# Kernel tuning notes

Measured on AMD Instinct MI355X. Metric: run time of the kernel, lower is better.

The kernel has to match this reference:

```python
import jax, jax.numpy as jnp
import numpy as np

N = 100  # n_subcritics; +-1/+-10 neighbor offsets imply a fixed 10x10 grid
OFFSETS = np.array([0, -10, 1, 10, -1])  # neighbor order: (i, i-10, i+1, i+10, i-1)


def _neighbor_gather(x):
    # x: [B, T, N, 7] -> xi: [B, T, N, 35]; out-of-range neighbors contribute zeros
    idx = np.arange(N)[:, None] + OFFSETS[None, :]          # [N, 5]
    mask = (idx >= 0) & (idx < N)
    idx_c = np.clip(idx, 0, N - 1)
    g = x[:, :, idx_c, :] * jnp.asarray(mask, x.dtype)[None, None, :, :, None]
    return g.reshape(x.shape[0], x.shape[1], N, 5 * x.shape[-1])


def _forward(x, lm_W1, lm_b1, lm_W2, lm_b2, lm_W3, lm_b3,
             gru_Wih, gru_Whh, gru_bih, gru_bhh,
             sc_W1, sc_b1, sc_W2, sc_b2, sc_W3, sc_b3):
    xi = _neighbor_gather(x)                                 # [B, T, N, 35]
    # LocalizedModule (per-node MLP) on the last timestep
    xl = xi[:, -1]                                           # [B, N, 35]
    h = jax.nn.relu(jnp.einsum('bnf,nfh->bnh', xl, lm_W1) + lm_b1)
    h = jax.nn.relu(jnp.einsum('bnf,nfh->bnh', h, lm_W2) + lm_b2)
    f = jnp.einsum('bnf,nfo->bno', h, lm_W3) + lm_b3         # [B, N, 1]
    # SubCritic: per-node GRU (PyTorch gate order r, z, n) over time, then MLP on final hidden
    def step(hc, xt):
        gi = jnp.einsum('bnf,ngf->bng', xt, gru_Wih) + gru_bih   # [B, N, 48]
        gh = jnp.einsum('bnh,ngh->bng', hc, gru_Whh) + gru_bhh
        ir, iz, i_n = jnp.split(gi, 3, axis=-1)
        hr, hz, h_n = jnp.split(gh, 3, axis=-1)
        r = jax.nn.sigmoid(ir + hr)
        z = jax.nn.sigmoid(iz + hz)
        n = jnp.tanh(i_n + r * h_n)
        return (1.0 - z) * n + z * hc, None
    h0 = jnp.zeros((x.shape[0], N, gru_Whh.shape[-1]), x.dtype)
    hT, _ = jax.lax.scan(step, h0, jnp.moveaxis(xi, 1, 0))   # final hidden [B, N, 16]
    g = jax.nn.relu(jnp.einsum('bnf,nfh->bnh', hT, sc_W1) + sc_b1)
    g = jax.nn.relu(jnp.einsum('bnf,nfh->bnh', g, sc_W2) + sc_b2)
    q = jnp.einsum('bnf,nfo->bno', g, sc_W3) + sc_b3         # [B, N, 1]
    # torch.cat over node-major lists of [B,1] then sum(dim=1) -> [N*B]
    return jnp.transpose(f[..., 0] + q[..., 0]).reshape(-1)


def setup_inputs():
    key = jax.random.key(0)
    ks = jax.random.split(key, 18)
    B, T, S, G = 128, 256, 7, 16
    def w(k, shape, scale=0.05):
        return jax.random.normal(k, shape, dtype=jnp.float32) * scale
    return {
        'x': jax.random.normal(ks[0], (B, T, N, S), dtype=jnp.float32),
        'lm_W1': w(ks[1], (N, 35, 512)), 'lm_b1': w(ks[2], (N, 512)),
        'lm_W2': w(ks[3], (N, 512, 256)), 'lm_b2': w(ks[4], (N, 256)),
        'lm_W3': w(ks[5], (N, 256, 1)), 'lm_b3': w(ks[6], (N, 1)),
        'gru_Wih': w(ks[7], (N, 3 * G, 35)), 'gru_Whh': w(ks[8], (N, 3 * G, G)),
        'gru_bih': w(ks[9], (N, 3 * G)), 'gru_bhh': w(ks[10], (N, 3 * G)),
        'sc_W1': w(ks[11], (N, G, G)), 'sc_b1': w(ks[12], (N, G)),
        'sc_W2': w(ks[13], (N, G, G)), 'sc_b2': w(ks[14], (N, G)),
        'sc_W3': w(ks[15], (N, G, 1)), 'sc_b3': w(ks[16], (N, 1)),
    }


def reference(x, lm_W1, lm_b1, lm_W2, lm_b2, lm_W3, lm_b3,
              gru_Wih, gru_Whh, gru_bih, gru_bhh,
              sc_W1, sc_b1, sc_W2, sc_b2, sc_W3, sc_b3):
    return _forward(x, lm_W1, lm_b1, lm_W2, lm_b2, lm_W3, lm_b3,
                    gru_Wih, gru_Whh, gru_bih, gru_bhh,
                    sc_W1, sc_b1, sc_W2, sc_b2, sc_W3, sc_b3)
```

## Files before the change

kernel.cpp:

```cpp
#include <hip/hip_runtime.h>
#include <cstddef>

#define NN 100
#define TT 256
#define BB 128
#define SS 7
#define FF 35
#define GG 16

typedef __attribute__((ext_vector_type(4))) float f32x4;
typedef __attribute__((ext_vector_type(8))) short short8;

__constant__ int c_off[5] = {0, -10, 1, 10, -1};

__device__ __forceinline__ float sigmoidf_(float v) {
  return __builtin_amdgcn_rcpf(1.0f + __expf(-v));
}
__device__ __forceinline__ float tanhf_(float v) {
  return 1.0f - 2.0f * __builtin_amdgcn_rcpf(__expf(2.0f * v) + 1.0f);
}
__device__ __forceinline__ unsigned bf1(float a) {
  unsigned u = __float_as_uint(a);
  return (u + 0x7FFFu + ((u >> 16) & 1u)) >> 16;
}
__device__ __forceinline__ unsigned bfp(float lo, float hi) {
  return bf1(lo) | (bf1(hi) << 16);
}
__device__ __forceinline__ unsigned pkt(float lo, float hi) {
  return (__float_as_uint(lo) >> 16) | (__float_as_uint(hi) & 0xFFFF0000u);
}

__global__ void __launch_bounds__(512)
k_lm1(const float* __restrict__ x, const float* __restrict__ W1,
      const float* __restrict__ b1, float* __restrict__ H1) {
  const int bc = blockIdx.x;
  const int n  = blockIdx.y;
  const int b0 = bc * 32;
  const int tid = threadIdx.x;
  __shared__ __align__(16) float xl[32][36];
  for (int idx = tid; idx < 32 * FF; idx += 512) {
    const int bb = idx / FF, f = idx % FF;
    const int m = n + c_off[f / SS];
    const int s = f % SS;
    float v = 0.0f;
    if (m >= 0 && m < NN)
      v = x[(((size_t)(b0 + bb) * TT + (TT - 1)) * NN + m) * SS + s];
    xl[bb][f] = v;
  }
  __syncthreads();
  const int h = tid;
  float w[FF];
  const float* wp = W1 + (size_t)n * FF * 512 + h;
#pragma unroll
  for (int f = 0; f < FF; ++f) w[f] = wp[(size_t)f * 512];
  const float bias = b1[n * 512 + h];
  for (int bb = 0; bb < 32; ++bb) {
    const float4* xr = (const float4*)(&xl[bb][0]);
    float acc = bias;
#pragma unroll
    for (int q = 0; q < 8; ++q) {
      const float4 v = xr[q];
      acc += w[4*q+0] * v.x + w[4*q+1] * v.y + w[4*q+2] * v.z + w[4*q+3] * v.w;
    }
    {
      const float4 v = xr[8];
      acc += w[32] * v.x + w[33] * v.y + w[34] * v.z;
    }
    H1[((size_t)(b0 + bb) * NN + n) * 512 + h] = fmaxf(acc, 0.0f);
  }
}

__global__ void __launch_bounds__(256)
k_lm2(const float* __restrict__ H1, const float* __restrict__ W2,
      const float* __restrict__ bias2, float* __restrict__ H2) {
  const int w  = threadIdx.x >> 6;
  const int l  = threadIdx.x & 63;
  const int n  = blockIdx.x >> 5;
  const int tg = blockIdx.x & 31;
  const int tau = tg * 4 + w;
  const int rt = tau >> 4;
  const int ct = tau & 15;
  const int lr = l & 15;
  const int kg = l >> 4;

  const int arow = rt * 16 + lr;
  const int col  = ct * 16 + lr;

  const float* Ab = H1 + ((size_t)arow * NN + n) * 512 + kg * 8;
  const float* Bb = W2 + (size_t)n * 512 * 256 + (size_t)(kg * 8) * 256 + col;

  f32x4 acc = {0.0f, 0.0f, 0.0f, 0.0f};
#pragma unroll 2
  for (int k0 = 0; k0 < 512; k0 += 32) {
    const float4 a0 = *(const float4*)(Ab + k0);
    const float4 a1 = *(const float4*)(Ab + k0 + 4);
    const float* bp = Bb + (size_t)k0 * 256;
    const float w0 = bp[0],    w1 = bp[256],  w2 = bp[512],  w3 = bp[768];
    const float w4 = bp[1024], w5 = bp[1280], w6 = bp[1536], w7 = bp[1792];
    union { short8 s; unsigned u[4]; } A, B;
    A.u[0] = pkt(a0.x, a0.y); A.u[1] = pkt(a0.z, a0.w);
    A.u[2] = pkt(a1.x, a1.y); A.u[3] = pkt(a1.z, a1.w);
    B.u[0] = pkt(w0, w1); B.u[1] = pkt(w2, w3);
    B.u[2] = pkt(w4, w5); B.u[3] = pkt(w6, w7);
    acc = __builtin_amdgcn_mfma_f32_16x16x32_bf16(A.s, B.s, acc, 0, 0, 0);
  }
  const float bv = bias2[n * 256 + col];
#pragma unroll
  for (int r = 0; r < 4; ++r) {
    const int grow = rt * 16 + kg * 4 + r;
    H2[((size_t)grow * NN + n) * 256 + col] = fmaxf(acc[r] + bv, 0.0f);
  }
}

__global__ void __launch_bounds__(256)
k_lm3(const float* __restrict__ H2, const float* __restrict__ W3,
      const float* __restrict__ b3, float* __restrict__ out) {
  const int w = threadIdx.x >> 6;
  const int lane = threadIdx.x & 63;
  const int p = blockIdx.x * 4 + w;
  const int b = p / NN, n = p % NN;
  const float4 hv = *(const float4*)(&H2[((size_t)b * NN + n) * 256 + lane*4]);
  const float4 wv = *(const float4*)(&W3[n * 256 + lane*4]);
  float dot = hv.x*wv.x + hv.y*wv.y + hv.z*wv.z + hv.w*wv.w;
#pragma unroll
  for (int off = 32; off > 0; off >>= 1) dot += __shfl_down(dot, off);
  if (lane == 0) out[n * BB + b] = dot + b3[n];
}

__device__ __forceinline__ float dot16s(const float4 u0, const float4 u1,
                                        const float4 u2, const float4 u3,
                                        const float4 h0, const float4 h1,
                                        const float4 h2, const float4 h3) {
  const float p0 = u0.x*h0.x + u0.y*h0.y + u0.z*h0.z + u0.w*h0.w;
  const float p1 = u1.x*h1.x + u1.y*h1.y + u1.z*h1.z + u1.w*h1.w;
  const float p2 = u2.x*h2.x + u2.y*h2.y + u2.z*h2.z + u2.w*h2.w;
  const float p3 = u3.x*h3.x + u3.y*h3.y + u3.z*h3.z + u3.w*h3.w;
  return (p0 + p1) + (p2 + p3);
}

__global__ void __launch_bounds__(64, 3)
k_gru(const float* __restrict__ x,
      const float* __restrict__ Wih, const float* __restrict__ Whh,
      const float* __restrict__ bih, const float* __restrict__ bhh,
      const float* __restrict__ sW1, const float* __restrict__ sb1,
      const float* __restrict__ sW2, const float* __restrict__ sb2,
      const float* __restrict__ sW3, const float* __restrict__ sb3,
      float* __restrict__ out) {
  const int l  = threadIdx.x;
  const int g  = l & 15;
  const int b  = l >> 4;
  const int kg = b;
  const int ab = (l & 15) >> 2;
  const int atoff = l & 3;
  const int bc = blockIdx.x;
  const int n  = blockIdx.y;
  const int bga = bc*4 + ab;
  const int bgp = bc*4 + b;

  __shared__ float hlds[4][16];

  const float* wh = Whh + ((size_t)n*48 + g)*GG;
  const float4 ur0 = *(const float4*)(wh+0),  ur1 = *(const float4*)(wh+4),
               ur2 = *(const float4*)(wh+8),  ur3 = *(const float4*)(wh+12);
  const float4 uz0 = *(const float4*)(wh+256),  uz1 = *(const float4*)(wh+260),
               uz2 = *(const float4*)(wh+264),  uz3 = *(const float4*)(wh+268);
  const float4 un0 = *(const float4*)(wh+512),  un1 = *(const float4*)(wh+516),
               un2 = *(const float4*)(wh+520),  un3 = *(const float4*)(wh+524);
  const float bir = bih[n*48 + g], biz = bih[n*48 + 16 + g], bin_ = bih[n*48 + 32 + g];
  const float bhr = bhh[n*48 + g], bhz = bhh[n*48 + 16 + g], bhn = bhh[n*48 + 32 + g];

  short8 bw[3], bw2[3];
#pragma unroll
  for (int c = 0; c < 3; ++c) {
    const float* wp = Wih + ((size_t)n*48 + c*16 + g)*FF;
    float t0_[8], t1_[8];
#pragma unroll
    for (int j = 0; j < 8; ++j) t0_[j] = wp[kg*8 + j];
#pragma unroll
    for (int j = 0; j < 8; ++j) {
      const int k2 = 32 + kg*8 + j;
      t1_[j] = (k2 < FF) ? wp[k2] : 0.0f;
    }
    union { short8 s; unsigned u[4]; } U, V;
#pragma unroll
    for (int jj = 0; jj < 4; ++jj) { U.u[jj] = bfp(t0_[2*jj], t0_[2*jj+1]);
                                     V.u[jj] = bfp(t1_[2*jj], t1_[2*jj+1]); }
    bw[c] = U.s; bw2[c] = V.s;
  }

  int adelta[8]; unsigned amask = 0;
#pragma unroll
  for (int j = 0; j < 8; ++j) {
    const int f  = kg*8 + j;
    const int fi = (f * 586) >> 12;
    const int s  = f - fi*7;
    const int mo = (fi == 0) ? 0 : (fi == 1) ? -10 : (fi == 2) ? 1 : (fi == 3) ? 10 : -1;
    adelta[j] = mo*SS + s;
    const int m = n + mo;
    if (m >= 0 && m < NN) amask |= (1u << j);
  }
  const bool v2 = (kg == 0) && (n >= 1);

  float xv[8], xv2[3];
  {
    const float* xq = x + ((size_t)bga*TT + atoff)*(NN*SS) + n*SS;
#pragma unroll
    for (int j = 0; j < 8; ++j) xv[j] = ((amask >> j) & 1u) ? xq[adelta[j]] : 0.0f;
#pragma unroll
    for (int j = 0; j < 3; ++j) xv2[j] = v2 ? xq[-3 + j] : 0.0f;
  }

  hlds[b][g] = 0.0f;
  float hown = 0.0f;

  const f32x4 z4 = {0.0f, 0.0f, 0.0f, 0.0f};

  for (int rd = 0; rd < TT/4; ++rd) {
    union { short8 s; unsigned u[4]; } A1, A2;
#pragma unroll
    for (int jj = 0; jj < 4; ++jj) A1.u[jj] = pkt(xv[2*jj], xv[2*jj+1]);
    A2.u[0] = pkt(xv2[0], xv2[1]); A2.u[1] = pkt(xv2[2], 0.0f); A2.u[2] = 0; A2.u[3] = 0;
    const short8 af1 = A1.s, af2 = A2.s;

    if (rd < TT/4 - 1) {
      const float* xq = x + ((size_t)bga*TT + (rd*4 + 4 + atoff))*(NN*SS) + n*SS;
#pragma unroll
      for (int j = 0; j < 8; ++j) xv[j] = ((amask >> j) & 1u) ? xq[adelta[j]] : 0.0f;
#pragma unroll
      for (int j = 0; j < 3; ++j) xv2[j] = v2 ? xq[-3 + j] : 0.0f;
    }

    f32x4 c0 = __builtin_amdgcn_mfma_f32_16x16x32_bf16(af1, bw[0], z4, 0, 0, 0);
    c0 = __builtin_amdgcn_mfma_f32_16x16x32_bf16(af2, bw2[0], c0, 0, 0, 0);
    f32x4 c1 = __builtin_amdgcn_mfma_f32_16x16x32_bf16(af1, bw[1], z4, 0, 0, 0);
    c1 = __builtin_amdgcn_mfma_f32_16x16x32_bf16(af2, bw2[1], c1, 0, 0, 0);
    f32x4 c2 = __builtin_amdgcn_mfma_f32_16x16x32_bf16(af1, bw[2], z4, 0, 0, 0);
    c2 = __builtin_amdgcn_mfma_f32_16x16x32_bf16(af2, bw2[2], c2, 0, 0, 0);

#pragma unroll
    for (int toff = 0; toff < 4; ++toff) {
      const float ir  = c0[toff] + bir;
      const float iz  = c1[toff] + biz;
      const float in_ = c2[toff] + bin_;
      const float4* hp = (const float4*)(&hlds[b][0]);
      const float4 h0 = hp[0], h1 = hp[1], h2 = hp[2], h3 = hp[3];
      const float hr = bhr + dot16s(ur0, ur1, ur2, ur3, h0, h1, h2, h3);
      const float hz = bhz + dot16s(uz0, uz1, uz2, uz3, h0, h1, h2, h3);
      const float hn = bhn + dot16s(un0, un1, un2, un3, h0, h1, h2, h3);
      const float r   = sigmoidf_(ir + hr);
      const float z   = sigmoidf_(iz + hz);
      const float nn2 = tanhf_(in_ + r * hn);
      const float hnew = nn2 + z * (hown - nn2);
      hlds[b][g] = hnew;
      hown = hnew;
    }
  }

  {
    const float4* hp = (const float4*)(&hlds[b][0]);
    const float4 h0 = hp[0], h1 = hp[1], h2 = hp[2], h3 = hp[3];
    const float* w1 = sW1 + n*GG*GG + g;
    float a1 = sb1[n*GG + g];
    a1 += h0.x*w1[0*GG] + h0.y*w1[1*GG] + h0.z*w1[2*GG] + h0.w*w1[3*GG];
    a1 += h1.x*w1[4*GG] + h1.y*w1[5*GG] + h1.z*w1[6*GG] + h1.w*w1[7*GG];
    a1 += h2.x*w1[8*GG] + h2.y*w1[9*GG] + h2.z*w1[10*GG] + h2.w*w1[11*GG];
    a1 += h3.x*w1[12*GG] + h3.y*w1[13*GG] + h3.z*w1[14*GG] + h3.w*w1[15*GG];
    a1 = fmaxf(a1, 0.0f);
    hlds[b][g] = a1;
  }
  {
    const float4* hp = (const float4*)(&hlds[b][0]);
    const float4 h0 = hp[0], h1 = hp[1], h2 = hp[2], h3 = hp[3];
    const float* w2 = sW2 + n*GG*GG + g;
    float a2 = sb2[n*GG + g];
    a2 += h0.x*w2[0*GG] + h0.y*w2[1*GG] + h0.z*w2[2*GG] + h0.w*w2[3*GG];
    a2 += h1.x*w2[4*GG] + h1.y*w2[5*GG] + h1.z*w2[6*GG] + h1.w*w2[7*GG];
    a2 += h2.x*w2[8*GG] + h2.y*w2[9*GG] + h2.z*w2[10*GG] + h2.w*w2[11*GG];
    a2 += h3.x*w2[12*GG] + h3.y*w2[13*GG] + h3.z*w2[14*GG] + h3.w*w2[15*GG];
    a2 = fmaxf(a2, 0.0f);
    float p = a2 * sW3[n*GG + g];
    p += __shfl_xor(p, 1);
    p += __shfl_xor(p, 2);
    p += __shfl_xor(p, 4);
    p += __shfl_xor(p, 8);
    if (g == 0) out[n * BB + bgp] += p + sb3[n];
  }
}

extern "C" void kernel_launch(void* const* d_in, const int* in_sizes, int n_in,
                              void* d_out, int out_size, void* d_ws, size_t ws_size,
                              hipStream_t stream) {
  const float* x     = (const float*)d_in[0];
  const float* lm_W1 = (const float*)d_in[1];
  const float* lm_b1 = (const float*)d_in[2];
  const float* lm_W2 = (const float*)d_in[3];
  const float* lm_b2 = (const float*)d_in[4];
  const float* lm_W3 = (const float*)d_in[5];
  const float* lm_b3 = (const float*)d_in[6];
  const float* gWih  = (const float*)d_in[7];
  const float* gWhh  = (const float*)d_in[8];
  const float* gbih  = (const float*)d_in[9];
  const float* gbhh  = (const float*)d_in[10];
  const float* sW1   = (const float*)d_in[11];
  const float* sb1   = (const float*)d_in[12];
  const float* sW2   = (const float*)d_in[13];
  const float* sb2   = (const float*)d_in[14];
  const float* sW3   = (const float*)d_in[15];
  const float* sb3   = (const float*)d_in[16];
  float* out = (float*)d_out;

  float* H1 = (float*)d_ws;
  float* H2 = (float*)((char*)d_ws + (size_t)BB * NN * 512 * 4);

  k_lm1<<<dim3(4, NN), 512, 0, stream>>>(x, lm_W1, lm_b1, H1);
  k_lm2<<<dim3(3200), 256, 0, stream>>>(H1, lm_W2, lm_b2, H2);
  k_lm3<<<dim3(3200), 256, 0, stream>>>(H2, lm_W3, lm_b3, out);
  k_gru<<<dim3(32, NN), 64, 0, stream>>>(x, gWih, gWhh, gbih, gbhh,
                                         sW1, sb1, sW2, sb2, sW3, sb3, out);
}
```

Baseline: 542.4 us.

## Tile lm2 GEMM through shared memory and broadcast GRU hidden state via DPP

```diff
diff --git a/kernel.cpp b/kernel.cpp
--- a/kernel.cpp
+++ b/kernel.cpp
@@ -29,6 +29,10 @@
 __device__ __forceinline__ unsigned pkt(float lo, float hi) {
   return (__float_as_uint(lo) >> 16) | (__float_as_uint(hi) & 0xFFFF0000u);
 }
+
+#define RORF(dst, src, J)                                                     \
+  dst = __uint_as_float(__builtin_amdgcn_update_dpp(                          \
+      0, (int)__float_as_uint(src), 0x120 + (J), 0xF, 0xF, true));
 
 __global__ void __launch_bounds__(512)
 k_lm1(const float* __restrict__ x, const float* __restrict__ W1,
@@ -73,42 +77,64 @@
 __global__ void __launch_bounds__(256)
 k_lm2(const float* __restrict__ H1, const float* __restrict__ W2,
       const float* __restrict__ bias2, float* __restrict__ H2) {
-  const int w  = threadIdx.x >> 6;
-  const int l  = threadIdx.x & 63;
-  const int n  = blockIdx.x >> 5;
-  const int tg = blockIdx.x & 31;
-  const int tau = tg * 4 + w;
-  const int rt = tau >> 4;
-  const int ct = tau & 15;
+  const int n  = blockIdx.x;
+  const int bh = blockIdx.y >> 2;
+  const int ch = blockIdx.y & 3;
+  const int t  = threadIdx.x;
+  const int w  = t >> 6;
+  const int l  = t & 63;
   const int lr = l & 15;
   const int kg = l >> 4;
-
-  const int arow = rt * 16 + lr;
-  const int col  = ct * 16 + lr;
-
-  const float* Ab = H1 + ((size_t)arow * NN + n) * 512 + kg * 8;
-  const float* Bb = W2 + (size_t)n * 512 * 256 + (size_t)(kg * 8) * 256 + col;
-
-  f32x4 acc = {0.0f, 0.0f, 0.0f, 0.0f};
-#pragma unroll 2
-  for (int k0 = 0; k0 < 512; k0 += 32) {
-    const float4 a0 = *(const float4*)(Ab + k0);
-    const float4 a1 = *(const float4*)(Ab + k0 + 4);
-    const float* bp = Bb + (size_t)k0 * 256;
-    const float w0 = bp[0],    w1 = bp[256],  w2 = bp[512],  w3 = bp[768];
-    const float w4 = bp[1024], w5 = bp[1280], w6 = bp[1536], w7 = bp[1792];
-    union { short8 s; unsigned u[4]; } A, B;
-    A.u[0] = pkt(a0.x, a0.y); A.u[1] = pkt(a0.z, a0.w);
-    A.u[2] = pkt(a1.x, a1.y); A.u[3] = pkt(a1.z, a1.w);
-    B.u[0] = pkt(w0, w1); B.u[1] = pkt(w2, w3);
-    B.u[2] = pkt(w4, w5); B.u[3] = pkt(w6, w7);
-    acc = __builtin_amdgcn_mfma_f32_16x16x32_bf16(A.s, B.s, acc, 0, 0, 0);
-  }
-  const float bv = bias2[n * 256 + col];
+  const int m0 = (w >> 1) * 32;
+  const int c0 = (w & 1) * 32;
+
+  __shared__ __align__(16) unsigned short As[64][72];
+
+  f32x4 acc00 = {0,0,0,0}, acc01 = {0,0,0,0}, acc10 = {0,0,0,0}, acc11 = {0,0,0,0};
+
+  const int colg0 = ch * 64 + c0;
+  const float* Bbase = W2 + (size_t)n * 512 * 256;
+
+  for (int k0 = 0; k0 < 512; k0 += 64) {
+    __syncthreads();
+#pragma unroll
+    for (int q = 0; q < 4; ++q) {
+      const int idx = t + q * 256;
+      const int row = idx >> 4;
+      const int kq  = idx & 15;
+      const float4 v = *(const float4*)(&H1[((size_t)(bh*64 + row) * NN + n) * 512 + k0 + kq*4]);
+      uint2 pv; pv.x = pkt(v.x, v.y); pv.y = pkt(v.z, v.w);
+      *(uint2*)(&As[row][kq*4]) = pv;
+    }
+    __syncthreads();
+#pragma unroll
+    for (int kc = 0; kc < 2; ++kc) {
+      const short8 a0 = *(const short8*)(&As[m0 + lr][kc*32 + kg*8]);
+      const short8 a1 = *(const short8*)(&As[m0 + 16 + lr][kc*32 + kg*8]);
+      union { short8 s; unsigned u[4]; } B0, B1;
+      const float* bp0 = Bbase + (size_t)(k0 + kc*32 + kg*8) * 256 + colg0 + lr;
+      const float* bp1 = bp0 + 16;
+#pragma unroll
+      for (int jj = 0; jj < 4; ++jj) {
+        B0.u[jj] = pkt(bp0[(size_t)(2*jj)*256], bp0[(size_t)(2*jj+1)*256]);
+        B1.u[jj] = pkt(bp1[(size_t)(2*jj)*256], bp1[(size_t)(2*jj+1)*256]);
+      }
+      acc00 = __builtin_amdgcn_mfma_f32_16x16x32_bf16(a0, B0.s, acc00, 0, 0, 0);
+      acc01 = __builtin_amdgcn_mfma_f32_16x16x32_bf16(a0, B1.s, acc01, 0, 0, 0);
+      acc10 = __builtin_amdgcn_mfma_f32_16x16x32_bf16(a1, B0.s, acc10, 0, 0, 0);
+      acc11 = __builtin_amdgcn_mfma_f32_16x16x32_bf16(a1, B1.s, acc11, 0, 0, 0);
+    }
+  }
+  const int colA = colg0 + lr, colB = colA + 16;
+  const float bva = bias2[n*256 + colA], bvb = bias2[n*256 + colB];
 #pragma unroll
   for (int r = 0; r < 4; ++r) {
-    const int grow = rt * 16 + kg * 4 + r;
-    H2[((size_t)grow * NN + n) * 256 + col] = fmaxf(acc[r] + bv, 0.0f);
+    const int rowA = bh*64 + m0 + kg*4 + r;
+    const int rowB = rowA + 16;
+    H2[((size_t)rowA * NN + n) * 256 + colA] = fmaxf(acc00[r] + bva, 0.0f);
+    H2[((size_t)rowA * NN + n) * 256 + colB] = fmaxf(acc01[r] + bvb, 0.0f);
+    H2[((size_t)rowB * NN + n) * 256 + colA] = fmaxf(acc10[r] + bva, 0.0f);
+    H2[((size_t)rowB * NN + n) * 256 + colB] = fmaxf(acc11[r] + bvb, 0.0f);
   }
 }
 
@@ -125,17 +151,6 @@
 #pragma unroll
   for (int off = 32; off > 0; off >>= 1) dot += __shfl_down(dot, off);
   if (lane == 0) out[n * BB + b] = dot + b3[n];
-}
-
-__device__ __forceinline__ float dot16s(const float4 u0, const float4 u1,
-                                        const float4 u2, const float4 u3,
-                                        const float4 h0, const float4 h1,
-                                        const float4 h2, const float4 h3) {
-  const float p0 = u0.x*h0.x + u0.y*h0.y + u0.z*h0.z + u0.w*h0.w;
-  const float p1 = u1.x*h1.x + u1.y*h1.y + u1.z*h1.z + u1.w*h1.w;
-  const float p2 = u2.x*h2.x + u2.y*h2.y + u2.z*h2.z + u2.w*h2.w;
-  const float p3 = u3.x*h3.x + u3.y*h3.y + u3.z*h3.z + u3.w*h3.w;
-  return (p0 + p1) + (p2 + p3);
 }
 
 __global__ void __launch_bounds__(64, 3)
@@ -157,15 +172,18 @@
   const int bga = bc*4 + ab;
   const int bgp = bc*4 + b;
 
-  __shared__ float hlds[4][16];
-
-  const float* wh = Whh + ((size_t)n*48 + g)*GG;
-  const float4 ur0 = *(const float4*)(wh+0),  ur1 = *(const float4*)(wh+4),
-               ur2 = *(const float4*)(wh+8),  ur3 = *(const float4*)(wh+12);
-  const float4 uz0 = *(const float4*)(wh+256),  uz1 = *(const float4*)(wh+260),
-               uz2 = *(const float4*)(wh+264),  uz3 = *(const float4*)(wh+268);
-  const float4 un0 = *(const float4*)(wh+512),  un1 = *(const float4*)(wh+516),
-               un2 = *(const float4*)(wh+520),  un3 = *(const float4*)(wh+524);
+  const int wpr = __builtin_amdgcn_update_dpp(0, g, 0x121, 0xF, 0xF, true);
+  const int s   = (wpr == ((g + 15) & 15)) ? -1 : 1;
+
+  const float* whr = Whh + ((size_t)n*48 +      g) * GG;
+  const float* whz = Whh + ((size_t)n*48 + 16 + g) * GG;
+  const float* whn = Whh + ((size_t)n*48 + 32 + g) * GG;
+  float ur[16], uz[16], un[16];
+#pragma unroll
+  for (int j = 0; j < 16; ++j) {
+    const int ix = (g + s*j) & 15;
+    ur[j] = whr[ix]; uz[j] = whz[ix]; un[j] = whn[ix];
+  }
   const float bir = bih[n*48 + g], biz = bih[n*48 + 16 + g], bin_ = bih[n*48 + 32 + g];
   const float bhr = bhh[n*48 + g], bhz = bhh[n*48 + 16 + g], bhn = bhh[n*48 + 32 + g];
 
@@ -181,11 +199,11 @@
       const int k2 = 32 + kg*8 + j;
       t1_[j] = (k2 < FF) ? wp[k2] : 0.0f;
     }
-    union { short8 s; unsigned u[4]; } U, V;
+    union { short8 s8; unsigned u[4]; } U, V;
 #pragma unroll
     for (int jj = 0; jj < 4; ++jj) { U.u[jj] = bfp(t0_[2*jj], t0_[2*jj+1]);
                                      V.u[jj] = bfp(t1_[2*jj], t1_[2*jj+1]); }
-    bw[c] = U.s; bw2[c] = V.s;
+    bw[c] = U.s8; bw2[c] = V.s8;
   }
 
   int adelta[8]; unsigned amask = 0;
@@ -193,9 +211,9 @@
   for (int j = 0; j < 8; ++j) {
     const int f  = kg*8 + j;
     const int fi = (f * 586) >> 12;
-    const int s  = f - fi*7;
+    const int sg = f - fi*7;
     const int mo = (fi == 0) ? 0 : (fi == 1) ? -10 : (fi == 2) ? 1 : (fi == 3) ? 10 : -1;
-    adelta[j] = mo*SS + s;
+    adelta[j] = mo*SS + sg;
     const int m = n + mo;
     if (m >= 0 && m < NN) amask |= (1u << j);
   }
@@ -210,17 +228,15 @@
     for (int j = 0; j < 3; ++j) xv2[j] = v2 ? xq[-3 + j] : 0.0f;
   }
 
-  hlds[b][g] = 0.0f;
   float hown = 0.0f;
-
   const f32x4 z4 = {0.0f, 0.0f, 0.0f, 0.0f};
 
   for (int rd = 0; rd < TT/4; ++rd) {
-    union { short8 s; unsigned u[4]; } A1, A2;
+    union { short8 s8; unsigned u[4]; } A1, A2;
 #pragma unroll
     for (int jj = 0; jj < 4; ++jj) A1.u[jj] = pkt(xv[2*jj], xv[2*jj+1]);
     A2.u[0] = pkt(xv2[0], xv2[1]); A2.u[1] = pkt(xv2[2], 0.0f); A2.u[2] = 0; A2.u[3] = 0;
-    const short8 af1 = A1.s, af2 = A2.s;
+    const short8 af1 = A1.s8, af2 = A2.s8;
 
     if (rd < TT/4 - 1) {
       const float* xq = x + ((size_t)bga*TT + (rd*4 + 4 + atoff))*(NN*SS) + n*SS;
@@ -239,45 +255,75 @@
 
 #pragma unroll
     for (int toff = 0; toff < 4; ++toff) {
-      const float ir  = c0[toff] + bir;
-      const float iz  = c1[toff] + biz;
-      const float in_ = c2[toff] + bin_;
-      const float4* hp = (const float4*)(&hlds[b][0]);
-      const float4 h0 = hp[0], h1 = hp[1], h2 = hp[2], h3 = hp[3];
-      const float hr = bhr + dot16s(ur0, ur1, ur2, ur3, h0, h1, h2, h3);
-      const float hz = bhz + dot16s(uz0, uz1, uz2, uz3, h0, h1, h2, h3);
-      const float hn = bhn + dot16s(un0, un1, un2, un3, h0, h1, h2, h3);
-      const float r   = sigmoidf_(ir + hr);
-      const float z   = sigmoidf_(iz + hz);
-      const float nn2 = tanhf_(in_ + r * hn);
-      const float hnew = nn2 + z * (hown - nn2);
-      hlds[b][g] = hnew;
-      hown = hnew;
-    }
-  }
-
+      float h1, h2, h3, h4, h5, h6, h7, h8, h9, h10, h11, h12, h13, h14, h15;
+      RORF(h1,  hown, 1)  RORF(h2,  hown, 2)  RORF(h3,  hown, 3)
+      RORF(h4,  hown, 4)  RORF(h5,  hown, 5)  RORF(h6,  hown, 6)
+      RORF(h7,  hown, 7)  RORF(h8,  hown, 8)  RORF(h9,  hown, 9)
+      RORF(h10, hown, 10) RORF(h11, hown, 11) RORF(h12, hown, 12)
+      RORF(h13, hown, 13) RORF(h14, hown, 14) RORF(h15, hown, 15)
+
+      float pr0 = ur[0]*hown + ur[1]*h1  + ur[2]*h2  + ur[3]*h3;
+      float pr1 = ur[4]*h4   + ur[5]*h5  + ur[6]*h6  + ur[7]*h7;
+      float pr2 = ur[8]*h8   + ur[9]*h9  + ur[10]*h10 + ur[11]*h11;
+      float pr3 = ur[12]*h12 + ur[13]*h13 + ur[14]*h14 + ur[15]*h15;
+      const float hr = bhr + ((pr0 + pr1) + (pr2 + pr3));
+
+      float pz0 = uz[0]*hown + uz[1]*h1  + uz[2]*h2  + uz[3]*h3;
+      float pz1 = uz[4]*h4   + uz[5]*h5  + uz[6]*h6  + uz[7]*h7;
+      float pz2 = uz[8]*h8   + uz[9]*h9  + uz[10]*h10 + uz[11]*h11;
+      float pz3 = uz[12]*h12 + uz[13]*h13 + uz[14]*h14 + uz[15]*h15;
+      const float hz = bhz + ((pz0 + pz1) + (pz2 + pz3));
+
+      float pn0 = un[0]*hown + un[1]*h1  + un[2]*h2  + un[3]*h3;
+      float pn1 = un[4]*h4   + un[5]*h5  + un[6]*h6  + un[7]*h7;
+      float pn2 = un[8]*h8   + un[9]*h9  + un[10]*h10 + un[11]*h11;
+      float pn3 = un[12]*h12 + un[13]*h13 + un[14]*h14 + un[15]*h15;
+      const float hn = bhn + ((pn0 + pn1) + (pn2 + pn3));
+
+      const float r   = sigmoidf_(c0[toff] + bir + hr);
+      const float z   = sigmoidf_(c1[toff] + biz + hz);
+      const float nn2 = tanhf_(c2[toff] + bin_ + r * hn);
+      hown = nn2 + z * (hown - nn2);
+    }
+  }
+
+  float a1;
   {
-    const float4* hp = (const float4*)(&hlds[b][0]);
-    const float4 h0 = hp[0], h1 = hp[1], h2 = hp[2], h3 = hp[3];
-    const float* w1 = sW1 + n*GG*GG + g;
-    float a1 = sb1[n*GG + g];
-    a1 += h0.x*w1[0*GG] + h0.y*w1[1*GG] + h0.z*w1[2*GG] + h0.w*w1[3*GG];
-    a1 += h1.x*w1[4*GG] + h1.y*w1[5*GG] + h1.z*w1[6*GG] + h1.w*w1[7*GG];
-    a1 += h2.x*w1[8*GG] + h2.y*w1[9*GG] + h2.z*w1[10*GG] + h2.w*w1[11*GG];
-    a1 += h3.x*w1[12*GG] + h3.y*w1[13*GG] + h3.z*w1[14*GG] + h3.w*w1[15*GG];
-    a1 = fmaxf(a1, 0.0f);
-    hlds[b][g] = a1;
-  }
+    float h1, h2, h3, h4, h5, h6, h7, h8, h9, h10, h11, h12, h13, h14, h15;
+    RORF(h1,  hown, 1)  RORF(h2,  hown, 2)  RORF(h3,  hown, 3)
+    RORF(h4,  hown, 4)  RORF(h5,  hown, 5)  RORF(h6,  hown, 6)
+    RORF(h7,  hown, 7)  RORF(h8,  hown, 8)  RORF(h9,  hown, 9)
+    RORF(h10, hown, 10) RORF(h11, hown, 11) RORF(h12, hown, 12)
+    RORF(h13, hown, 13) RORF(h14, hown, 14) RORF(h15, hown, 15)
+    const float* w1 = sW1 + n*GG*GG;
+    float acc = sb1[n*GG + g];
+    const float hv[16] = {hown,h1,h2,h3,h4,h5,h6,h7,h8,h9,h10,h11,h12,h13,h14,h15};
+#pragma unroll
+    for (int j = 0; j < 16; ++j) {
+      const int ix = (g + s*j) & 15;
+      acc += hv[j] * w1[ix*GG + g];
+    }
+    a1 = fmaxf(acc, 0.0f);
+  }
+  float a2;
   {
-    const float4* hp = (const float4*)(&hlds[b][0]);
-    const float4 h0 = hp[0], h1 = hp[1], h2 = hp[2], h3 = hp[3];
-    const float* w2 = sW2 + n*GG*GG + g;
-    float a2 = sb2[n*GG + g];
-    a2 += h0.x*w2[0*GG] + h0.y*w2[1*GG] + h0.z*w2[2*GG] + h0.w*w2[3*GG];
-    a2 += h1.x*w2[4*GG] + h1.y*w2[5*GG] + h1.z*w2[6*GG] + h1.w*w2[7*GG];
-    a2 += h2.x*w2[8*GG] + h2.y*w2[9*GG] + h2.z*w2[10*GG] + h2.w*w2[11*GG];
-    a2 += h3.x*w2[12*GG] + h3.y*w2[13*GG] + h3.z*w2[14*GG] + h3.w*w2[15*GG];
-    a2 = fmaxf(a2, 0.0f);
+    float h1, h2, h3, h4, h5, h6, h7, h8, h9, h10, h11, h12, h13, h14, h15;
+    RORF(h1,  a1, 1)  RORF(h2,  a1, 2)  RORF(h3,  a1, 3)
+    RORF(h4,  a1, 4)  RORF(h5,  a1, 5)  RORF(h6,  a1, 6)
+    RORF(h7,  a1, 7)  RORF(h8,  a1, 8)  RORF(h9,  a1, 9)
+    RORF(h10, a1, 10) RORF(h11, a1, 11) RORF(h12, a1, 12)
+    RORF(h13, a1, 13) RORF(h14, a1, 14) RORF(h15, a1, 15)
+    const float* w2 = sW2 + n*GG*GG;
+    float acc = sb2[n*GG + g];
+    const float hv[16] = {a1,h1,h2,h3,h4,h5,h6,h7,h8,h9,h10,h11,h12,h13,h14,h15};
+#pragma unroll
+    for (int j = 0; j < 16; ++j) {
+      const int ix = (g + s*j) & 15;
+      acc += hv[j] * w2[ix*GG + g];
+    }
+    a2 = fmaxf(acc, 0.0f);
+  }
+  {
     float p = a2 * sW3[n*GG + g];
     p += __shfl_xor(p, 1);
     p += __shfl_xor(p, 2);
@@ -313,7 +359,7 @@
   float* H2 = (float*)((char*)d_ws + (size_t)BB * NN * 512 * 4);
 
   k_lm1<<<dim3(4, NN), 512, 0, stream>>>(x, lm_W1, lm_b1, H1);
-  k_lm2<<<dim3(3200), 256, 0, stream>>>(H1, lm_W2, lm_b2, H2);
+  k_lm2<<<dim3(NN, 8), 256, 0, stream>>>(H1, lm_W2, lm_b2, H2);
   k_lm3<<<dim3(3200), 256, 0, stream>>>(H2, lm_W3, lm_b3, out);
   k_gru<<<dim3(32, NN), 64, 0, stream>>>(x, gWih, gWhh, gbih, gbhh,
                                          sW1, sb1, sW2, sb2, sW3, sb3, out);
```

Measured after the change: 490.9 us. 1.1x faster.
